# Optimization experiments

Measured on AMD Instinct MI355X. Metric: run time of the kernel, lower is better.

Reference implementation:

```python
import jax, jax.numpy as jnp
import numpy as np

DIM = 768
N_HEADS = 12
HEAD_DIM = DIM // N_HEADS
MLP_DIM = 3072
DEPTH = 12
B, N = 16, 512


def setup_inputs() -> dict:
    key = jax.random.key(0)
    ks = jax.random.split(key, 12)
    s = 0.02
    return {
        "x": jax.random.normal(ks[0], (B, N, DIM), dtype=jnp.float32),
        "ln_w": jnp.ones((DIM,), jnp.float32),
        "ln_b": jnp.zeros((DIM,), jnp.float32),
        "wq": jax.random.normal(ks[1], (DIM, DIM), jnp.float32) * s,
        "bq": jnp.zeros((DIM,), jnp.float32),
        "wk": jax.random.normal(ks[2], (DIM, DIM), jnp.float32) * s,
        "bk": jnp.zeros((DIM,), jnp.float32),
        "wv": jax.random.normal(ks[3], (DIM, DIM), jnp.float32) * s,
        "bv": jnp.zeros((DIM,), jnp.float32),
        "w1": jax.random.normal(ks[4], (DIM, MLP_DIM), jnp.float32) * s,
        "b1": jnp.zeros((MLP_DIM,), jnp.float32),
        "w2": jax.random.normal(ks[5], (MLP_DIM, DIM), jnp.float32) * s,
        "b2": jnp.zeros((DIM,), jnp.float32),
    }


def _layernorm(x, w, b):
    mu = jnp.mean(x, axis=-1, keepdims=True)
    var = jnp.var(x, axis=-1, keepdims=True)
    return (x - mu) * jax.lax.rsqrt(var + 1e-5) * w + b


def _mha(x, wq, bq, wk, bk, wv, bv):
    # x: [b, n, dim]; weights stored as [in, out]
    def heads(t):
        return t.reshape(B, N, N_HEADS, HEAD_DIM).transpose(0, 2, 1, 3)  # b h n d
    q = heads(x @ wq + bq)
    k = heads(x @ wk + bk)
    v = heads(x @ wv + bv)
    scores = jnp.einsum('bhqd,bhkd->bhqk', q, k) / np.sqrt(HEAD_DIM).astype(np.float32)
    attn = jax.nn.softmax(scores, axis=-1)
    o = jnp.einsum('bhqk,bhkd->bhqd', attn, v)
    return o.transpose(0, 2, 1, 3).reshape(B, N, DIM)


def reference(x, ln_w, ln_b, wq, bq, wk, bk, wv, bv, w1, b1, w2, b2):
    # Dropout is identity in eval mode. Same weights reused each depth iteration.
    for _ in range(DEPTH):
        x = _mha(_layernorm(x, ln_w, ln_b), wq, bq, wk, bk, wv, bv) + x
        h = _layernorm(x, ln_w, ln_b)
        h = jax.nn.gelu(h @ w1 + b1, approximate=False) @ w2 + b2
        x = h + x
    return x
```

## Files before the change

kernel.cpp:

```cpp
#include <hip/hip_runtime.h>

typedef __bf16 bf16x8 __attribute__((ext_vector_type(8)));
typedef float f32x4 __attribute__((ext_vector_type(4)));
typedef unsigned short ushort8_t __attribute__((ext_vector_type(8)));
typedef unsigned short ushort4_t __attribute__((ext_vector_type(4)));

#define MFMA16(a, b, c) __builtin_amdgcn_mfma_f32_16x16x32_bf16((a), (b), (c), 0, 0, 0)

#define GLOAD16(gp, lp)                                                        \
  __builtin_amdgcn_global_load_lds(                                            \
      (__attribute__((address_space(1))) void*)(gp),                           \
      (__attribute__((address_space(3))) void*)(lp), 16, 0, 0)

__device__ __forceinline__ unsigned short f2bf(float f) {
  unsigned u = __builtin_bit_cast(unsigned, f);
  return (unsigned short)((u + 0x7FFFu + ((u >> 16) & 1u)) >> 16);
}

__global__ __launch_bounds__(256) void transpose_f2b(
    const float* __restrict__ src, unsigned short* __restrict__ dst,
    int Kdim, int Ndim) {
  long i = (long)blockIdx.x * 256 + threadIdx.x;
  if (i >= (long)Kdim * Ndim) return;
  int n = (int)(i / Kdim);
  int kk = (int)(i - (long)n * Kdim);
  dst[i] = f2bf(src[(long)kk * Ndim + n]);
}

__global__ __launch_bounds__(256) void ln_kernel(
    const float* __restrict__ x, const float* __restrict__ gw,
    const float* __restrict__ gb, unsigned short* __restrict__ h) {
  const int row = blockIdx.x * 4 + (threadIdx.x >> 6);
  const int l = threadIdx.x & 63;
  const float* xr = x + (long)row * 768;
  f32x4 va[3];
#pragma unroll
  for (int i = 0; i < 3; i++) va[i] = *(const f32x4*)(xr + i * 256 + l * 4);
  float s = 0.f, ss = 0.f;
#pragma unroll
  for (int i = 0; i < 3; i++)
#pragma unroll
    for (int j = 0; j < 4; j++) {
      float t = va[i][j];
      s += t;
      ss += t * t;
    }
#pragma unroll
  for (int off = 1; off < 64; off <<= 1) {
    s += __shfl_xor(s, off, 64);
    ss += __shfl_xor(ss, off, 64);
  }
  const float mu = s * (1.f / 768.f);
  const float var = ss * (1.f / 768.f) - mu * mu;
  const float inv = rsqrtf(var + 1e-5f);
  unsigned short* hp = h + (long)row * 768;
#pragma unroll
  for (int i = 0; i < 3; i++) {
    f32x4 wv = *(const f32x4*)(gw + i * 256 + l * 4);
    f32x4 bv = *(const f32x4*)(gb + i * 256 + l * 4);
    ushort4_t o;
#pragma unroll
    for (int j = 0; j < 4; j++) o[j] = f2bf((va[i][j] - mu) * inv * wv[j] + bv[j]);
    *(ushort4_t*)(hp + i * 256 + l * 4) = o;
  }
}

enum { EPI_QKV = 0, EPI_GELU = 1, EPI_RES = 2 };

template <int EPI, int MREP>
__global__ __launch_bounds__(256) void gemm_bt(
    const unsigned short* __restrict__ A, const unsigned short* __restrict__ BT,
    int K, const float* __restrict__ bb0, const float* __restrict__ bb1,
    const float* __restrict__ bb2, unsigned short* __restrict__ o0,
    unsigned short* __restrict__ o1, unsigned short* __restrict__ o2,
    const float* oFin, float* oFout) {
  constexpr int BM = MREP * 32;
  __shared__ unsigned short As[2][2][BM * 32];
  __shared__ unsigned short Bs[2][2][128 * 32];
  const int tid = threadIdx.x;
  const int w = tid >> 6, l = tid & 63;
  const int lr = l & 15, lg = l >> 4;
  const int wr = w >> 1, wc = w & 1;

  const int nx = gridDim.x;
  const int nwg = nx * gridDim.y;
  int wg = blockIdx.y * nx + blockIdx.x;
  {
    const int qq = nwg >> 3, rr = nwg & 7;
    const int xcd = wg & 7, idx = wg >> 3;
    wg = (xcd < rr ? xcd * (qq + 1) : rr * (qq + 1) + (xcd - rr) * qq) + idx;
  }
  const int bx = wg % nx, by = wg / nx;
  const int m0 = by * BM, n0 = bx * 128;

  const unsigned short* Ag = A + (long)(m0 + w * (BM / 4) + (l >> 2)) * K + (l & 3) * 8;
  const unsigned short* Bg = BT + (long)(n0 + w * 32 + (l >> 2)) * K + (l & 3) * 8;

  auto stage = [&](int buf, int kt) {
    const long ko = (long)kt * 64;
#pragma unroll
    for (int kk = 0; kk < 2; kk++) {
#pragma unroll
      for (int h = 0; h < BM / 64; h++)
        GLOAD16(Ag + (long)(h * 16) * K + ko + kk * 32,
                &As[buf][kk][(w * (BM / 4) + h * 16) * 32 + l * 8]);
#pragma unroll
      for (int h = 0; h < 2; h++)
        GLOAD16(Bg + (long)(h * 16) * K + ko + kk * 32,
                &Bs[buf][kk][(w * 32 + h * 16) * 32 + l * 8]);
    }
  };

  f32x4 acc[MREP][4] = {};
  const int nk = K >> 6;
  stage(0, 0);
  for (int kt = 0; kt < nk; ++kt) {
    const int cur = kt & 1;
    __syncthreads();
    if (kt + 1 < nk) stage(cur ^ 1, kt + 1);
#pragma unroll
    for (int kk = 0; kk < 2; kk++) {
      bf16x8 a[MREP], b[4];
#pragma unroll
      for (int i = 0; i < MREP; i++)
        a[i] = *(const bf16x8*)(&As[cur][kk][(wr * MREP * 16 + i * 16 + lr) * 32 + lg * 8]);
#pragma unroll
      for (int j = 0; j < 4; j++)
        b[j] = *(const bf16x8*)(&Bs[cur][kk][(wc * 64 + j * 16 + lr) * 32 + lg * 8]);
      __builtin_amdgcn_s_setprio(1);
#pragma unroll
      for (int i = 0; i < MREP; i++)
#pragma unroll
        for (int j = 0; j < 4; j++) acc[i][j] = MFMA16(a[i], b[j], acc[i][j]);
      __builtin_amdgcn_s_setprio(0);
    }
  }

  if (EPI == EPI_QKV) {
    const int whichq = n0 / 768;
    const int cc0 = n0 - whichq * 768;
    const float* bias = whichq == 0 ? bb0 : whichq == 1 ? bb1 : bb2;
    if (whichq < 2) {
      unsigned short* dst = whichq == 0 ? o0 : o1;
#pragma unroll
      for (int i = 0; i < MREP; i++) {
        const int r = m0 + wr * MREP * 16 + i * 16 + lg * 4;
#pragma unroll
        for (int j = 0; j < 4; j++) {
          const int ccol = cc0 + wc * 64 + j * 16 + lr;
          const int hd = ccol >> 6, d = ccol & 63;
          const float bv = bias[ccol];
#pragma unroll
          for (int q = 0; q < 4; q++) {
            const int row = r + q;
            const int bidx = row >> 9, n = row & 511;
            const long addr = ((long)(bidx * 12 + hd) * 512 + n) * 64 + d;
            dst[addr] = f2bf(acc[i][j][q] + bv);
          }
        }
      }
    } else {
#pragma unroll
      for (int i = 0; i < MREP; i++) {
        const int r = m0 + wr * MREP * 16 + i * 16 + lg * 4;
        const int bidx = r >> 9, nb = r & 511;
#pragma unroll
        for (int j = 0; j < 4; j++) {
          const int ccol = cc0 + wc * 64 + j * 16 + lr;
          const int hd = ccol >> 6, d = ccol & 63;
          const float bv = bias[ccol];
          ushort4_t pk;
#pragma unroll
          for (int q = 0; q < 4; q++) pk[q] = f2bf(acc[i][j][q] + bv);
          *(ushort4_t*)(&o2[((long)(bidx * 12 + hd) * 64 + d) * 512 + nb]) = pk;
        }
      }
    }
  } else if (EPI == EPI_GELU) {
#pragma unroll
    for (int i = 0; i < MREP; i++) {
      const int r = m0 + wr * MREP * 16 + i * 16 + lg * 4;
#pragma unroll
      for (int j = 0; j < 4; j++) {
        const int c = n0 + wc * 64 + j * 16 + lr;
        const float bv = bb0[c];
#pragma unroll
        for (int q = 0; q < 4; q++) {
          float v = acc[i][j][q] + bv;
          const float u = v * (0.7978845608f + 0.0356774081f * v * v);
          const float g = v / (1.0f + __expf(-2.0f * u));
          o0[(long)(r + q) * 3072 + c] = f2bf(g);
        }
      }
    }
  } else {
#pragma unroll
    for (int i = 0; i < MREP; i++) {
      const int r = m0 + wr * MREP * 16 + i * 16 + lg * 4;
#pragma unroll
      for (int j = 0; j < 4; j++) {
        const int c = n0 + wc * 64 + j * 16 + lr;
        const float bv = bb0[c];
#pragma unroll
        for (int q = 0; q < 4; q++) {
          const long addr = (long)(r + q) * 768 + c;
          oFout[addr] = acc[i][j][q] + bv + oFin[addr];
        }
      }
    }
  }
}

__global__ __launch_bounds__(256) void attn_kernel(
    const unsigned short* __restrict__ qg, const unsigned short* __restrict__ kg,
    const unsigned short* __restrict__ vtg, float* __restrict__ x) {
  __shared__ unsigned short Sh[128 * 64];
  __shared__ unsigned short Ks[2][64 * 64];
  __shared__ unsigned short Vt[2][64 * 64];
  const int qt = blockIdx.x, h = blockIdx.y, b = blockIdx.z;
  const int bh = b * 12 + h;
  const int tid = threadIdx.x, w = tid >> 6, l = tid & 63;
  const int lr = l & 15, lg = l >> 4;
  const int fchunk = ((l & 7) ^ ((l >> 3) & 7)) * 8;
  const int rk = lr & 7;

  const unsigned short* qbase =
      qg + ((long)bh * 512 + qt * 128 + w * 32 + (l >> 3)) * 64 + fchunk;
  unsigned short* shW = &Sh[w * 2048 + l * 8];
#pragma unroll
  for (int cc = 0; cc < 4; cc++) GLOAD16(qbase + cc * 8 * 64, shW + cc * 512);

  const unsigned short* kbase =
      kg + ((long)bh * 512 + w * 16 + (l >> 3)) * 64 + fchunk;
  const unsigned short* vbase =
      vtg + ((long)bh * 64 + w * 16 + (l >> 3)) * 512 + fchunk;
  unsigned short* KsW = &Ks[0][w * 1024 + l * 8];
  unsigned short* VtW = &Vt[0][w * 1024 + l * 8];

  auto stageKV = [&](int buf, int kt) {
#pragma unroll
    for (int cc = 0; cc < 2; cc++) {
      GLOAD16(kbase + (kt * 64 + cc * 8) * 64, KsW + buf * 4096 + cc * 512);
      GLOAD16(vbase + cc * 8 * 512 + kt * 64, VtW + buf * 4096 + cc * 512);
    }
  };
  stageKV(0, 0);
  __syncthreads();

  bf16x8 qa[2][2];
#pragma unroll
  for (int mi = 0; mi < 2; mi++)
#pragma unroll
    for (int ds = 0; ds < 2; ds++) {
      qa[mi][ds] = *(const bf16x8*)(&Sh[(w * 32 + mi * 16 + lr) * 64 +
                                        ((ds * 4 + lg) ^ rk) * 8]);
#pragma unroll
      for (int e = 0; e < 8; e++)
        qa[mi][ds][e] = (__bf16)(0.125f * (float)qa[mi][ds][e]);
    }

  unsigned short* Pw = &Sh[w * 2048];
  float lsum[8] = {};
  f32x4 o[2][4] = {};

  for (int kt = 0; kt < 8; ++kt) {
    const int cur = kt & 1;
    if (kt < 7) stageKV(cur ^ 1, kt + 1);

    f32x4 s[2][4] = {};
#pragma unroll
    for (int ds = 0; ds < 2; ++ds) {
      bf16x8 kb[4];
#pragma unroll
      for (int nj = 0; nj < 4; nj++)
        kb[nj] = *(const bf16x8*)(&Ks[cur][(nj * 16 + lr) * 64 +
                                           ((ds * 4 + lg) ^ rk) * 8]);
#pragma unroll
      for (int mi = 0; mi < 2; mi++)
#pragma unroll
        for (int nj = 0; nj < 4; nj++) s[mi][nj] = MFMA16(qa[mi][ds], kb[nj], s[mi][nj]);
    }

#pragma unroll
    for (int mi = 0; mi < 2; mi++)
#pragma unroll
      for (int nj = 0; nj < 4; nj++) {
        const int cL = nj * 2 + (lr >> 3);
#pragma unroll
        for (int q = 0; q < 4; q++) {
          const int row = mi * 16 + lg * 4 + q;
          const float p = __expf(s[mi][nj][q]);
          lsum[mi * 4 + q] += p;
          Pw[row * 64 + ((cL ^ (row & 7)) * 8) + (lr & 7)] = f2bf(p);
        }
      }

#pragma unroll
    for (int ks = 0; ks < 2; ++ks) {
      bf16x8 pa[2], vb[4];
#pragma unroll
      for (int mi = 0; mi < 2; mi++)
        pa[mi] = *(const bf16x8*)(&Pw[(mi * 16 + lr) * 64 +
                                      ((ks * 4 + lg) ^ rk) * 8]);
#pragma unroll
      for (int dj = 0; dj < 4; dj++)
        vb[dj] = *(const bf16x8*)(&Vt[cur][(dj * 16 + lr) * 64 +
                                           ((ks * 4 + lg) ^ rk) * 8]);
#pragma unroll
      for (int mi = 0; mi < 2; mi++)
#pragma unroll
        for (int dj = 0; dj < 4; dj++) o[mi][dj] = MFMA16(pa[mi], vb[dj], o[mi][dj]);
    }
    __syncthreads();
  }

#pragma unroll
  for (int i = 0; i < 8; i++) {
#pragma unroll
    for (int off = 1; off < 16; off <<= 1) lsum[i] += __shfl_xor(lsum[i], off, 64);
  }

#pragma unroll
  for (int mi = 0; mi < 2; mi++) {
#pragma unroll
    for (int q = 0; q < 4; q++) {
      const int n = qt * 128 + w * 32 + mi * 16 + lg * 4 + q;
      const float inv = 1.0f / lsum[mi * 4 + q];
      const long base = ((long)(b * 512 + n)) * 768 + h * 64;
#pragma unroll
      for (int dj = 0; dj < 4; dj++) {
        const long a = base + dj * 16 + lr;
        x[a] = x[a] + o[mi][dj][q] * inv;
      }
    }
  }
}

extern "C" void kernel_launch(void* const* d_in, const int* in_sizes, int n_in,
                              void* d_out, int out_size, void* d_ws,
                              size_t ws_size, hipStream_t stream) {
  const float* x_in = (const float*)d_in[0];
  const float* ln_w = (const float*)d_in[1];
  const float* ln_b = (const float*)d_in[2];
  const float* wq = (const float*)d_in[3];
  const float* bq = (const float*)d_in[4];
  const float* wk = (const float*)d_in[5];
  const float* bk = (const float*)d_in[6];
  const float* wv = (const float*)d_in[7];
  const float* bv = (const float*)d_in[8];
  const float* w1 = (const float*)d_in[9];
  const float* b1 = (const float*)d_in[10];
  const float* w2 = (const float*)d_in[11];
  const float* b2 = (const float*)d_in[12];

  char* p = (char*)d_ws;
  float* xw = (float*)p;            p += 8192L * 768 * 4;
  unsigned short* hbuf = (unsigned short*)p;  p += 8192L * 768 * 2;
  unsigned short* wqkvT = (unsigned short*)p; p += 2304L * 768 * 2;
  unsigned short* w1T = (unsigned short*)p;   p += 3072L * 768 * 2;
  unsigned short* w2T = (unsigned short*)p;   p += 768L * 3072 * 2;
  unsigned short* qb = (unsigned short*)p;
  unsigned short* kb = qb + 6291456L;
  unsigned short* vt = kb + 6291456L;
  unsigned short* gbuf = qb;

  hipMemcpyAsync(xw, x_in, 8192L * 768 * 4, hipMemcpyDeviceToDevice, stream);

  transpose_f2b<<<(768 * 768 + 255) / 256, 256, 0, stream>>>(wq, wqkvT, 768, 768);
  transpose_f2b<<<(768 * 768 + 255) / 256, 256, 0, stream>>>(wk, wqkvT + 589824L, 768, 768);
  transpose_f2b<<<(768 * 768 + 255) / 256, 256, 0, stream>>>(wv, wqkvT + 1179648L, 768, 768);
  transpose_f2b<<<(768 * 3072 + 255) / 256, 256, 0, stream>>>(w1, w1T, 768, 3072);
  transpose_f2b<<<(768 * 3072 + 255) / 256, 256, 0, stream>>>(w2, w2T, 3072, 768);

  for (int layer = 0; layer < 12; ++layer) {
    ln_kernel<<<2048, 256, 0, stream>>>(xw, ln_w, ln_b, hbuf);
    gemm_bt<EPI_QKV, 4><<<dim3(18, 64), 256, 0, stream>>>(
        hbuf, wqkvT, 768, bq, bk, bv, qb, kb, vt, nullptr, nullptr);
    attn_kernel<<<dim3(4, 12, 16), 256, 0, stream>>>(qb, kb, vt, xw);
    ln_kernel<<<2048, 256, 0, stream>>>(xw, ln_w, ln_b, hbuf);
    gemm_bt<EPI_GELU, 4><<<dim3(24, 64), 256, 0, stream>>>(
        hbuf, w1T, 768, b1, nullptr, nullptr, gbuf, nullptr, nullptr, nullptr,
        nullptr);
    gemm_bt<EPI_RES, 2><<<dim3(6, 128), 256, 0, stream>>>(
        gbuf, w2T, 3072, b2, nullptr, nullptr, nullptr, nullptr, nullptr, xw,
        layer == 11 ? (float*)d_out : xw);
  }
}
```

Measured before the change: 2.697 ms.

## Store GEMM operands in pre-tiled 16x32 blocks for contiguous LDS staging

The GEMM operands (LN output, GELU output and the transposed weights) now use a tiled layout in which each 16-row by 32-k block is a contiguous 512-element chunk. Each global_load_lds then moves one whole contiguous 1KB tile, and the LDS fragment reads become linear per lane. The producers (ln_kernel, the GELU epilogue and the weight transpose) write this tiled layout directly. The aim is fully coalesced global loads and fewer address computations in the GEMM main loop. In exchange the GELU epilogue now scatters 2-byte stores, and the LDS reads lose their previous row-stride pattern, which may change bank-conflict behaviour.

```diff
diff --git a/kernel.cpp b/kernel.cpp
--- a/kernel.cpp
+++ b/kernel.cpp
@@ -17,14 +17,23 @@
   return (unsigned short)((u + 0x7FFFu + ((u >> 16) & 1u)) >> 16);
 }
 
-__global__ __launch_bounds__(256) void transpose_f2b(
+
+__global__ __launch_bounds__(256) void transpose_f2b_tiled(
     const float* __restrict__ src, unsigned short* __restrict__ dst,
     int Kdim, int Ndim) {
-  long i = (long)blockIdx.x * 256 + threadIdx.x;
-  if (i >= (long)Kdim * Ndim) return;
-  int n = (int)(i / Kdim);
-  int kk = (int)(i - (long)n * Kdim);
-  dst[i] = f2bf(src[(long)kk * Ndim + n]);
+  const long u = (long)blockIdx.x * 256 + threadIdx.x;
+  const long total = ((long)Kdim * Ndim) >> 3;
+  if (u >= total) return;
+  const int kt32 = Kdim >> 5;
+  const long tile = u >> 6;
+  const int t8 = (int)(u & 63);
+  const int chunk = t8 >> 4, rowlow = t8 & 15;
+  const int n = (int)(tile / kt32) * 16 + rowlow;
+  const int k0 = (int)(tile % kt32) * 32 + chunk * 8;
+  ushort8_t o;
+#pragma unroll
+  for (int e = 0; e < 8; e++) o[e] = f2bf(src[(long)(k0 + e) * Ndim + n]);
+  *(ushort8_t*)(dst + (u << 3)) = o;
 }
 
 __global__ __launch_bounds__(256) void ln_kernel(
@@ -53,7 +62,9 @@
   const float mu = s * (1.f / 768.f);
   const float var = ss * (1.f / 768.f) - mu * mu;
   const float inv = rsqrtf(var + 1e-5f);
-  unsigned short* hp = h + (long)row * 768;
+  const long tb = ((long)(row >> 4) * 24) << 9;
+  const int rlow = (row & 15) * 8;
+  const int coff = ((l >> 1) & 3) * 128 + rlow + (l & 1) * 4;
 #pragma unroll
   for (int i = 0; i < 3; i++) {
     f32x4 wv = *(const f32x4*)(gw + i * 256 + l * 4);
@@ -61,7 +72,8 @@
     ushort4_t o;
 #pragma unroll
     for (int j = 0; j < 4; j++) o[j] = f2bf((va[i][j] - mu) * inv * wv[j] + bv[j]);
-    *(ushort4_t*)(hp + i * 256 + l * 4) = o;
+    const long addr = tb + ((long)(i * 8 + (l >> 3)) << 9) + coff;
+    *(ushort4_t*)(h + addr) = o;
   }
 }
 
@@ -75,8 +87,9 @@
     unsigned short* __restrict__ o1, unsigned short* __restrict__ o2,
     const float* oFin, float* oFout) {
   constexpr int BM = MREP * 32;
-  __shared__ unsigned short As[2][2][BM * 32];
-  __shared__ unsigned short Bs[2][2][128 * 32];
+  constexpr int AG = BM / 16;
+  __shared__ unsigned short As[2][2][AG * 512];
+  __shared__ unsigned short Bs[2][2][8 * 512];
   const int tid = threadIdx.x;
   const int w = tid >> 6, l = tid & 63;
   const int lr = l & 15, lg = l >> 4;
@@ -93,21 +106,26 @@
   const int bx = wg % nx, by = wg / nx;
   const int m0 = by * BM, n0 = bx * 128;
 
-  const unsigned short* Ag = A + (long)(m0 + w * (BM / 4) + (l >> 2)) * K + (l & 3) * 8;
-  const unsigned short* Bg = BT + (long)(n0 + w * 32 + (l >> 2)) * K + (l & 3) * 8;
+  const int nk32 = K >> 5;
+  const long abase = (long)(m0 >> 4) * nk32;
+  const long bbase = (long)(n0 >> 4) * nk32;
 
   auto stage = [&](int buf, int kt) {
-    const long ko = (long)kt * 64;
 #pragma unroll
     for (int kk = 0; kk < 2; kk++) {
-#pragma unroll
-      for (int h = 0; h < BM / 64; h++)
-        GLOAD16(Ag + (long)(h * 16) * K + ko + kk * 32,
-                &As[buf][kk][(w * (BM / 4) + h * 16) * 32 + l * 8]);
-#pragma unroll
-      for (int h = 0; h < 2; h++)
-        GLOAD16(Bg + (long)(h * 16) * K + ko + kk * 32,
-                &Bs[buf][kk][(w * 32 + h * 16) * 32 + l * 8]);
+      const int pk = kt * 2 + kk;
+#pragma unroll
+      for (int t = 0; t < AG / 4; t++) {
+        const int g = w + t * 4;
+        GLOAD16(A + ((abase + (long)g * nk32 + pk) << 9) + l * 8,
+                &As[buf][kk][g * 512 + l * 8]);
+      }
+#pragma unroll
+      for (int t = 0; t < 2; t++) {
+        const int g = w + t * 4;
+        GLOAD16(BT + ((bbase + (long)g * nk32 + pk) << 9) + l * 8,
+                &Bs[buf][kk][g * 512 + l * 8]);
+      }
     }
   };
 
@@ -123,10 +141,10 @@
       bf16x8 a[MREP], b[4];
 #pragma unroll
       for (int i = 0; i < MREP; i++)
-        a[i] = *(const bf16x8*)(&As[cur][kk][(wr * MREP * 16 + i * 16 + lr) * 32 + lg * 8]);
+        a[i] = *(const bf16x8*)(&As[cur][kk][(wr * MREP + i) * 512 + l * 8]);
 #pragma unroll
       for (int j = 0; j < 4; j++)
-        b[j] = *(const bf16x8*)(&Bs[cur][kk][(wc * 64 + j * 16 + lr) * 32 + lg * 8]);
+        b[j] = *(const bf16x8*)(&Bs[cur][kk][(wc * 4 + j) * 512 + l * 8]);
       __builtin_amdgcn_s_setprio(1);
 #pragma unroll
       for (int i = 0; i < MREP; i++)
@@ -184,12 +202,14 @@
       for (int j = 0; j < 4; j++) {
         const int c = n0 + wc * 64 + j * 16 + lr;
         const float bv = bb0[c];
+        const long cpart = ((long)(c >> 5) << 9) + ((c >> 3) & 3) * 128 + (c & 7);
 #pragma unroll
         for (int q = 0; q < 4; q++) {
+          const int row = r + q;
           float v = acc[i][j][q] + bv;
           const float u = v * (0.7978845608f + 0.0356774081f * v * v);
           const float g = v / (1.0f + __expf(-2.0f * u));
-          o0[(long)(r + q) * 3072 + c] = f2bf(g);
+          o0[(((long)(row >> 4) * 96) << 9) + cpart + (row & 15) * 8] = f2bf(g);
         }
       }
     }
@@ -366,11 +386,16 @@
 
   hipMemcpyAsync(xw, x_in, 8192L * 768 * 4, hipMemcpyDeviceToDevice, stream);
 
-  transpose_f2b<<<(768 * 768 + 255) / 256, 256, 0, stream>>>(wq, wqkvT, 768, 768);
-  transpose_f2b<<<(768 * 768 + 255) / 256, 256, 0, stream>>>(wk, wqkvT + 589824L, 768, 768);
-  transpose_f2b<<<(768 * 768 + 255) / 256, 256, 0, stream>>>(wv, wqkvT + 1179648L, 768, 768);
-  transpose_f2b<<<(768 * 3072 + 255) / 256, 256, 0, stream>>>(w1, w1T, 768, 3072);
-  transpose_f2b<<<(768 * 3072 + 255) / 256, 256, 0, stream>>>(w2, w2T, 3072, 768);
+  transpose_f2b_tiled<<<(768 * 768 / 8 + 255) / 256, 256, 0, stream>>>(
+      wq, wqkvT, 768, 768);
+  transpose_f2b_tiled<<<(768 * 768 / 8 + 255) / 256, 256, 0, stream>>>(
+      wk, wqkvT + 768L * 768, 768, 768);
+  transpose_f2b_tiled<<<(768 * 768 / 8 + 255) / 256, 256, 0, stream>>>(
+      wv, wqkvT + 2L * 768 * 768, 768, 768);
+  transpose_f2b_tiled<<<(768 * 3072 / 8 + 255) / 256, 256, 0, stream>>>(
+      w1, w1T, 768, 3072);
+  transpose_f2b_tiled<<<(768 * 3072 / 8 + 255) / 256, 256, 0, stream>>>(
+      w2, w2T, 3072, 768);
 
   for (int layer = 0; layer < 12; ++layer) {
     ln_kernel<<<2048, 256, 0, stream>>>(xw, ln_w, ln_b, hbuf);
```

Result: faster. 2.493 ms (-7.6%).
